# Optimization experiments

Measured on AMD Instinct MI355X. Metric: run time of the kernel, lower is better.

## Reference

```python
import jax, jax.numpy as jnp
import numpy as np

L, H, D, V, CTX = 4, 12, 768, 50257, 2048
HD = D // H
EPS = 1e-5


def setup_inputs() -> dict:
    key = jax.random.key(0)
    ks = jax.random.split(key, 24)
    s = 0.02
    inp = {
        "tokens": jax.random.randint(ks[0], (1, CTX), 0, V, dtype=jnp.int32),
        "vocab_embed": jax.random.normal(ks[1], (V, D), jnp.float32) * s,
        "pos_embed": jax.random.normal(ks[2], (CTX, D), jnp.float32) * s,
        # per-layer stacked params [L, ...]
        "ln1_g": jnp.ones((L, D), jnp.float32),
        "ln1_b": jnp.zeros((L, D), jnp.float32),
        "att_w": jax.random.normal(ks[3], (L, D, 3 * D), jnp.float32) * s,
        "att_b": jnp.zeros((L, 3 * D), jnp.float32),
        "attn_proj_w": jax.random.normal(ks[4], (L, D, D), jnp.float32) * (s / np.sqrt(2 * L)),
        "attn_proj_b": jnp.zeros((L, D), jnp.float32),
        "ln2_g": jnp.ones((L, D), jnp.float32),
        "ln2_b": jnp.zeros((L, D), jnp.float32),
        "fc_w": jax.random.normal(ks[5], (L, D, 4 * D), jnp.float32) * s,
        "fc_b": jnp.zeros((L, 4 * D), jnp.float32),
        "mlp_proj_w": jax.random.normal(ks[6], (L, 4 * D, D), jnp.float32) * (s / np.sqrt(2 * L)),
        "mlp_proj_b": jnp.zeros((L, D), jnp.float32),
        "lnf_g": jnp.ones((D,), jnp.float32),
        "lnf_b": jnp.zeros((D,), jnp.float32),
        "out_w": jax.random.normal(ks[7], (D, V), jnp.float32) * s,
        "out_b": jnp.zeros((V,), jnp.float32),
    }
    return inp


def _layernorm(x, g, b):
    mu = jnp.mean(x, axis=-1, keepdims=True)
    var = jnp.mean(jnp.square(x - mu), axis=-1, keepdims=True)
    return (x - mu) * jax.lax.rsqrt(var + EPS) * g + b


def _gelu(x):
    # exact tanh-approx GELU as in the torch module
    c = np.sqrt(2.0 / np.pi).astype(np.float32)
    return x * 0.5 * (1.0 + jnp.tanh(c * (x + 0.044715 * x * x * x)))


def _forward(tokens, p):
    B, C = tokens.shape
    x = p["vocab_embed"][tokens] + p["pos_embed"][:C][None]  # [B,C,D]
    causal = jnp.tril(jnp.ones((C, C), bool))  # [C,C]
    scale = 1.0 / np.sqrt(HD)
    for l in range(L):
        h = _layernorm(x, p["ln1_g"][l], p["ln1_b"][l])
        qkv = h @ p["att_w"][l] + p["att_b"][l]
        q, k, v = jnp.split(qkv, 3, axis=-1)
        q = q.reshape(B, C, H, HD)
        k = k.reshape(B, C, H, HD)
        v = v.reshape(B, C, H, HD)
        att = jnp.einsum("bqhd,bkhd->bhqk", q, k) * scale
        att = jnp.where(causal[None, None], att, -jnp.inf)
        att = jax.nn.softmax(att, axis=-1)
        o = jnp.einsum("bhqk,bkhd->bqhd", att, v).reshape(B, C, D)
        x = h + (o @ p["attn_proj_w"][l] + p["attn_proj_b"][l])
        h2 = _layernorm(x, p["ln2_g"][l], p["ln2_b"][l])
        mlp = _gelu(h2 @ p["fc_w"][l] + p["fc_b"][l]) @ p["mlp_proj_w"][l] + p["mlp_proj_b"][l]
        x = h2 + mlp
    x = _layernorm(x, p["lnf_g"], p["lnf_b"])
    return x @ p["out_w"] + p["out_b"]  # [B,C,V]


def reference(tokens, vocab_embed, pos_embed, ln1_g, ln1_b, att_w, att_b,
              attn_proj_w, attn_proj_b, ln2_g, ln2_b, fc_w, fc_b,
              mlp_proj_w, mlp_proj_b, lnf_g, lnf_b, out_w, out_b):
    p = dict(vocab_embed=vocab_embed, pos_embed=pos_embed, ln1_g=ln1_g, ln1_b=ln1_b,
             att_w=att_w, att_b=att_b, attn_proj_w=attn_proj_w, attn_proj_b=attn_proj_b,
             ln2_g=ln2_g, ln2_b=ln2_b, fc_w=fc_w, fc_b=fc_b,
             mlp_proj_w=mlp_proj_w, mlp_proj_b=mlp_proj_b,
             lnf_g=lnf_g, lnf_b=lnf_b, out_w=out_w, out_b=out_b)
    return _forward(tokens, p)
```

## Files before the change

kernel.cpp:

```cpp
#include <hip/hip_runtime.h>
#include <hip/hip_bf16.h>
#include <math.h>

#define LAYERS 4
#define NHEAD  12
#define DMODEL 768
#define HEADD  64
#define NCTX   2048
#define NVOCAB 50257
#define NVPAD  50432
#define D3     (3*DMODEL)
#define D4     (4*DMODEL)

typedef short short8 __attribute__((ext_vector_type(8)));
typedef float f32x4  __attribute__((ext_vector_type(4)));
typedef float f32x4u __attribute__((ext_vector_type(4), aligned(4)));
typedef ushort ushx4 __attribute__((ext_vector_type(4)));

__device__ __forceinline__ float bf2f(ushort u) {
    union { uint i; float f; } c; c.i = ((uint)u) << 16; return c.f;
}
__device__ __forceinline__ ushort f2bf(float f) {
    union { float f; uint i; } c; c.f = f;
    uint i = c.i;
    uint r = (i + 0x7FFFu + ((i >> 16) & 1u)) >> 16;
    return (ushort)r;
}

#define GLD16(gp, lp) __builtin_amdgcn_global_load_lds( \
    (__attribute__((address_space(1))) void*)(gp),      \
    (__attribute__((address_space(3))) void*)(lp), 16, 0, 0)

__global__ void embed_k(const int* __restrict__ tok,
                        const float* __restrict__ ve,
                        const float* __restrict__ pe,
                        float* __restrict__ x) {
    int c = blockIdx.x;
    int t = tok[c];
    for (int d = threadIdx.x; d < DMODEL; d += blockDim.x)
        x[(size_t)c * DMODEL + d] = ve[(size_t)t * DMODEL + d] + pe[(size_t)c * DMODEL + d];
}

__global__ __launch_bounds__(256) void ln_v2(const float* __restrict__ x,
                                             const float* __restrict__ g,
                                             const float* __restrict__ b,
                                             float* __restrict__ yf,
                                             ushort* __restrict__ ybf) {
    const int w = threadIdx.x >> 6, l = threadIdx.x & 63;
    const int row = blockIdx.x * 4 + w;
    const float* xr = x + (size_t)row * DMODEL;

    f32x4 v[3];
    float s = 0.f, ss = 0.f;
    #pragma unroll
    for (int i = 0; i < 3; i++) {
        v[i] = *(const f32x4*)(xr + (l + 64 * i) * 4);
        #pragma unroll
        for (int k = 0; k < 4; k++) { s += v[i][k]; ss += v[i][k] * v[i][k]; }
    }
    #pragma unroll
    for (int off = 32; off > 0; off >>= 1) {
        s  += __shfl_xor(s, off);
        ss += __shfl_xor(ss, off);
    }
    const float mu = s * (1.f / DMODEL);
    const float var = ss * (1.f / DMODEL) - mu * mu;
    const float rstd = rsqrtf(var + 1e-5f);

    #pragma unroll
    for (int i = 0; i < 3; i++) {
        const int idx = l + 64 * i;
        f32x4 g4 = *(const f32x4*)(g + idx * 4);
        f32x4 b4 = *(const f32x4*)(b + idx * 4);
        f32x4 r;
        #pragma unroll
        for (int k = 0; k < 4; k++) r[k] = (v[i][k] - mu) * rstd * g4[k] + b4[k];
        if (yf) *(f32x4*)(yf + (size_t)row * DMODEL + idx * 4) = r;
        if (ybf) {
            ushx4 u;
            #pragma unroll
            for (int k = 0; k < 4; k++) u[k] = f2bf(r[k]);
            *(ushx4*)(ybf + (size_t)row * DMODEL + idx * 4) = u;
        }
    }
}

__global__ __launch_bounds__(256) void transp_bf16(const float* __restrict__ src,
                                                   ushort* __restrict__ dst,
                                                   int K, int N) {
    __shared__ float tile[32][33];
    const int nt = blockIdx.x * 32, kt = blockIdx.y * 32;
    const int t = threadIdx.x;
    const int lr = t >> 5, lc = t & 31;

    #pragma unroll
    for (int i = 0; i < 4; i++) {
        int k = kt + lr + i * 8, n = nt + lc;
        float v = (n < N) ? src[(size_t)k * N + n] : 0.f;
        tile[lr + i * 8][lc] = v;
    }
    __syncthreads();
    #pragma unroll
    for (int i = 0; i < 4; i++) {
        int n = nt + lr + i * 8, k = kt + lc;
        dst[(size_t)n * K + k] = f2bf(tile[lc][lr + i * 8]);
    }
}

__global__ __launch_bounds__(256) void transp4(
    const float* __restrict__ s0, const float* __restrict__ s1,
    const float* __restrict__ s2, const float* __restrict__ s3,
    ushort* __restrict__ d0, ushort* __restrict__ d1,
    ushort* __restrict__ d2, ushort* __restrict__ d3)
{
    __shared__ float tile[32][33];
    const int bid = blockIdx.x;
    const float* src; ushort* dst; int K, N, nx, tb;
    if (bid < 1728)      { src = s0; dst = d0; K = 768;  N = 2304; nx = 72; tb = bid; }
    else if (bid < 2304) { src = s1; dst = d1; K = 768;  N = 768;  nx = 24; tb = bid - 1728; }
    else if (bid < 4608) { src = s2; dst = d2; K = 768;  N = 3072; nx = 96; tb = bid - 2304; }
    else                 { src = s3; dst = d3; K = 3072; N = 768;  nx = 24; tb = bid - 4608; }
    const int nt = (tb % nx) * 32, kt = (tb / nx) * 32;
    const int t = threadIdx.x;
    const int lr = t >> 5, lc = t & 31;

    #pragma unroll
    for (int i = 0; i < 4; i++) {
        int k = kt + lr + i * 8, n = nt + lc;
        tile[lr + i * 8][lc] = src[(size_t)k * N + n];
    }
    __syncthreads();
    #pragma unroll
    for (int i = 0; i < 4; i++) {
        int n = nt + lr + i * 8, k = kt + lc;
        dst[(size_t)n * K + k] = f2bf(tile[lc][lr + i * 8]);
    }
}

template<int MT, int ACT, bool HASADD, bool OUTBF>
__global__ __launch_bounds__(256) void gemm3(
    const ushort* __restrict__ A, const ushort* __restrict__ Bt,
    const float* __restrict__ bias, const float* __restrict__ addsrc,
    void* __restrict__ Cout, int N, int K)
{
    constexpr int AFR  = MT / 32;
    constexpr int ABYT = MT * 64;
    constexpr int BUF  = ABYT + 8192;
    constexpr int LPS  = MT / 64 + 2;
    __shared__ __align__(16) char smem[3 * BUF];
    const int bm = blockIdx.y * MT, bn = blockIdx.x * 128;
    const int t = threadIdx.x, l = t & 63, w = t >> 6;
    const int wrb = (w >> 1) * (MT / 2), wcb = (w & 1) * 64;
    const int l15 = l & 15, lg = l >> 4;
    const int swr = ((l15 >> 1) & 3) << 4;

    const int srow = t >> 2;
    const int ssc  = ((t & 3) ^ ((srow >> 1) & 3)) * 8;
    const ushort* Abase = A  + (size_t)(bm + srow) * K + ssc;
    const ushort* Bbase = Bt + (size_t)(bn + srow) * K + ssc;

    f32x4 acc[AFR][4];
    #pragma unroll
    for (int i = 0; i < AFR; i++)
        #pragma unroll
        for (int j = 0; j < 4; j++) acc[i][j] = (f32x4)0.f;

    auto STAGE = [&](int buf, int ke) {
        ushort* as = (ushort*)(smem + buf * BUF);
        ushort* bs = (ushort*)(smem + buf * BUF + ABYT);
        #pragma unroll
        for (int i = 0; i < MT / 64; i++)
            GLD16(Abase + (size_t)i * 64 * K + ke, as + (t + i * 256) * 8);
        #pragma unroll
        for (int i = 0; i < 2; i++)
            GLD16(Bbase + (size_t)i * 64 * K + ke, bs + (t + i * 256) * 8);
    };
    auto COMPUTE = [&](int buf) {
        const char* as = smem + buf * BUF;
        const char* bs = smem + buf * BUF + ABYT;
        short8 af[AFR], bfr[4];
        #pragma unroll
        for (int f = 0; f < AFR; f++)
            af[f] = *(const short8*)(as + (((wrb + f * 16 + l15) * 64 + lg * 16) ^ swr));
        #pragma unroll
        for (int f = 0; f < 4; f++)
            bfr[f] = *(const short8*)(bs + (((wcb + f * 16 + l15) * 64 + lg * 16) ^ swr));
        __builtin_amdgcn_s_setprio(1);
        #pragma unroll
        for (int fm = 0; fm < AFR; fm++)
            #pragma unroll
            for (int fn = 0; fn < 4; fn++)
                acc[fm][fn] = __builtin_amdgcn_mfma_f32_16x16x32_bf16(
                    af[fm], bfr[fn], acc[fm][fn], 0, 0, 0);
        __builtin_amdgcn_s_setprio(0);
    };

    const int nk = K >> 5;
    STAGE(0, 0);
    STAGE(1, 32);
    int bc = 0, bs2 = 2;
    for (int kt = 0; kt < nk; kt++) {
        if (kt < nk - 1)
            asm volatile("s_waitcnt vmcnt(%0)" :: "i"(LPS) : "memory");
        else
            asm volatile("s_waitcnt vmcnt(0)" ::: "memory");
        __builtin_amdgcn_s_barrier();
        asm volatile("" ::: "memory");
        if (kt + 2 < nk) STAGE(bs2, (kt + 2) << 5);
        COMPUTE(bc);
        bc  = (bc  == 2) ? 0 : bc  + 1;
        bs2 = (bs2 == 2) ? 0 : bs2 + 1;
    }

    #pragma unroll
    for (int fn = 0; fn < 4; fn++) {
        const int col = bn + wcb + fn * 16 + l15;
        const float bi = bias[col];
        #pragma unroll
        for (int fm = 0; fm < AFR; fm++) {
            #pragma unroll
            for (int j = 0; j < 4; j++) {
                const int row = bm + wrb + fm * 16 + lg * 4 + j;
                float v = acc[fm][fn][j] + bi;
                if (ACT == 1) {
                    float u = 0.7978845608028654f * (v + 0.044715f * v * v * v);
                    v = 0.5f * v * (1.f + tanhf(u));
                }
                if (HASADD) v += addsrc[(size_t)row * N + col];
                if (OUTBF) ((ushort*)Cout)[(size_t)row * N + col] = f2bf(v);
                else       ((float*) Cout)[(size_t)row * N + col] = v;
            }
        }
    }
}

__global__ __launch_bounds__(1024) void gemm_logits(
    const ushort* __restrict__ A, const ushort* __restrict__ Bt,
    const float* __restrict__ bias, float* __restrict__ Cout)
{
    __shared__ __align__(16) char smem[98304];
    float* Cs = (float*)smem;

    const int pid = (blockIdx.x & 7) * 197 + (blockIdx.x >> 3);
    const int np = pid >> 3, mt = pid & 7;
    const int bm = mt * 256, bn = np * 256;
    const int t = threadIdx.x, l = t & 63, w = t >> 6;
    const int wm = w >> 2, wn = w & 3;
    const int l15 = l & 15, lg = l >> 4;
    const int swr = ((l15 >> 1) & 3) << 4;

    const int sr  = t >> 2;
    const int ssc = ((t & 3) ^ ((sr >> 1) & 3)) * 8;
    const ushort* Ab = A  + (size_t)(bm + sr) * DMODEL + ssc;
    const ushort* Bb = Bt + (size_t)(bn + sr) * DMODEL + ssc;

    f32x4 acc[4][4];
    #pragma unroll
    for (int i = 0; i < 4; i++)
        #pragma unroll
        for (int j = 0; j < 4; j++) acc[i][j] = (f32x4)0.f;

    auto STAGE = [&](int buf, int ke) {
        ushort* as = (ushort*)(smem + buf * 32768);
        ushort* bs = (ushort*)(smem + buf * 32768 + 16384);
        GLD16(Ab + ke, as + t * 8);
        GLD16(Bb + ke, bs + t * 8);
    };
    auto COMPUTE = [&](int buf) {
        const char* as = smem + buf * 32768;
        const char* bs = smem + buf * 32768 + 16384;
        short8 bfr[4];
        #pragma unroll
        for (int f = 0; f < 4; f++) {
            const int r = wn * 64 + f * 16 + l15;
            bfr[f] = *(const short8*)(bs + ((r * 64 + lg * 16) ^ swr));
        }
        __builtin_amdgcn_s_setprio(1);
        #pragma unroll
        for (int fm = 0; fm < 4; fm++) {
            const int r = wm * 64 + fm * 16 + l15;
            short8 af = *(const short8*)(as + ((r * 64 + lg * 16) ^ swr));
            #pragma unroll
            for (int fn = 0; fn < 4; fn++)
                acc[fm][fn] = __builtin_amdgcn_mfma_f32_16x16x32_bf16(
                    af, bfr[fn], acc[fm][fn], 0, 0, 0);
        }
        __builtin_amdgcn_s_setprio(0);
    };

    STAGE(0, 0);
    STAGE(1, 32);
    #pragma unroll
    for (int kt = 0; kt < 24; kt++) {
        if (kt <= 22) asm volatile("s_waitcnt vmcnt(2)" ::: "memory");
        else          asm volatile("s_waitcnt vmcnt(0)" ::: "memory");
        __builtin_amdgcn_s_barrier();
        asm volatile("" ::: "memory");
        if (kt + 2 < 24) STAGE((kt + 2) % 3, (kt + 2) * 32);
        COMPUTE(kt % 3);
    }

    #pragma unroll
    for (int p = 0; p < 4; p++) {
        __syncthreads();
        if (wm == p) {
            #pragma unroll
            for (int fm = 0; fm < 4; fm++) {
                #pragma unroll
                for (int fn = 0; fn < 4; fn++) {
                    const int ccol = wn * 64 + fn * 16 + l15;
                    const int gcol = bn + ccol;
                    const float bi = (gcol < NVOCAB) ? bias[gcol] : 0.f;
                    #pragma unroll
                    for (int j = 0; j < 4; j++)
                        Cs[(fm * 16 + lg * 4 + j) * 256 + ccol] = acc[fm][fn][j] + bi;
                }
            }
        }
        __syncthreads();
        const int grow0 = bm + p * 64;
        #pragma unroll
        for (int i = 0; i < 4; i++) {
            const int idx = t + i * 1024;
            const int rr = idx >> 6, ch = idx & 63;
            f32x4 v = *(const f32x4*)(Cs + rr * 256 + ch * 4);
            float* dst = Cout + (size_t)(grow0 + rr) * NVOCAB + bn + ch * 4;
            if (bn + 256 <= NVOCAB) {
                *(f32x4u*)dst = v;
            } else {
                #pragma unroll
                for (int e = 0; e < 4; e++)
                    if (bn + ch * 4 + e < NVOCAB) dst[e] = v[e];
            }
        }
    }
}

#define QBLK  64
#define KVBLK 64
__global__ __launch_bounds__(256) void qkv_tiles_k(const ushort* __restrict__ qkv,
                                                   ushort* __restrict__ Kimg,
                                                   ushort* __restrict__ Vimg) {
    __shared__ __align__(16) ushort Vt_l[4096];
    const int h = blockIdx.x;
    const int kt = blockIdx.y;
    const int k0 = kt * KVBLK;
    const int t = threadIdx.x;
    ushort* kd = Kimg + ((size_t)h * (NCTX / KVBLK) + kt) * 4096;
    ushort* vd = Vimg + ((size_t)h * (NCTX / KVBLK) + kt) * 4096;

    #pragma unroll
    for (int i = 0; i < 2; i++) {
        const int c = t + i * 256;
        const int r = c >> 3, cc = c & 7;
        short8 kv8 = *(const short8*)(qkv + (size_t)(k0 + r) * D3 + DMODEL + h * HEADD + cc * 8);
        *(short8*)(kd + (((r * 8 + cc) ^ (r & 7)) * 8)) = kv8;
        short8 vv = *(const short8*)(qkv + (size_t)(k0 + r) * D3 + 2 * DMODEL + h * HEADD + cc * 8);
        #pragma unroll
        for (int j = 0; j < 8; j++) {
            const int d = cc * 8 + j;
            const int addr = (d * 128 + r * 2) ^ ((d & 7) << 4);
            *(ushort*)((char*)Vt_l + addr) = (ushort)vv[j];
        }
    }
    __syncthreads();
    #pragma unroll
    for (int i = 0; i < 2; i++) {
        const int c = t + i * 256;
        *(short8*)(vd + c * 8) = *(const short8*)(Vt_l + c * 8);
    }
}

__device__ __forceinline__ void attn_step(
    const short8 qf[2], f32x4 Of[4], float m_run[4], float l_run[4],
    const ushort* Kt, const ushort* Vt, char* pw,
    int k0, int q0, int maskTile, int w, int l15, int lg)
{
    const float scale = 0.125f;
    f32x4 S[4];
    __builtin_amdgcn_s_setprio(1);
    #pragma unroll
    for (int nf = 0; nf < 4; nf++) {
        f32x4 a = (f32x4)0.f;
        #pragma unroll
        for (int s = 0; s < 2; s++) {
            const int r = nf * 16 + l15;
            const int addr = (r * 128 + s * 64 + lg * 16) ^ ((r & 7) << 4);
            short8 kf = *(const short8*)((const char*)Kt + addr);
            a = __builtin_amdgcn_mfma_f32_16x16x32_bf16(qf[s], kf, a, 0, 0, 0);
        }
        S[nf] = a;
    }
    __builtin_amdgcn_s_setprio(0);

    float p[4][4];
    if (maskTile) {
        #pragma unroll
        for (int nf = 0; nf < 4; nf++) {
            const int kvg = k0 + nf * 16 + l15;
            #pragma unroll
            for (int j = 0; j < 4; j++) {
                const int qg = q0 + w * 16 + lg * 4 + j;
                p[nf][j] = (kvg <= qg) ? S[nf][j] * scale : -1e30f;
            }
        }
    } else {
        #pragma unroll
        for (int nf = 0; nf < 4; nf++)
            #pragma unroll
            for (int j = 0; j < 4; j++)
                p[nf][j] = S[nf][j] * scale;
    }

    #pragma unroll
    for (int j = 0; j < 4; j++) {
        float mx = fmaxf(fmaxf(p[0][j], p[1][j]), fmaxf(p[2][j], p[3][j]));
        mx = fmaxf(mx, __shfl_xor(mx, 1));
        mx = fmaxf(mx, __shfl_xor(mx, 2));
        mx = fmaxf(mx, __shfl_xor(mx, 4));
        mx = fmaxf(mx, __shfl_xor(mx, 8));
        const float mnew = fmaxf(m_run[j], mx);
        const float sc = __expf(m_run[j] - mnew);
        m_run[j] = mnew;
        float psum = 0.f;
        #pragma unroll
        for (int nf = 0; nf < 4; nf++) {
            const float e = __expf(p[nf][j] - mnew);
            p[nf][j] = e;
            psum += e;
        }
        psum += __shfl_xor(psum, 1);
        psum += __shfl_xor(psum, 2);
        psum += __shfl_xor(psum, 4);
        psum += __shfl_xor(psum, 8);
        l_run[j] = l_run[j] * sc + psum;
        #pragma unroll
        for (int df = 0; df < 4; df++) Of[df][j] *= sc;
    }

    #pragma unroll
    for (int nf = 0; nf < 4; nf++)
        #pragma unroll
        for (int j = 0; j < 4; j++) {
            const int ql = lg * 4 + j;
            const int addr = (ql * 128 + (nf * 16 + l15) * 2) ^ ((ql & 7) << 4);
            *(ushort*)(pw + addr) = f2bf(p[nf][j]);
        }

    __builtin_amdgcn_s_setprio(1);
    #pragma unroll
    for (int s = 0; s < 2; s++) {
        const int paddr = (l15 * 128 + s * 64 + lg * 16) ^ ((l15 & 7) << 4);
        short8 pf = *(const short8*)(pw + paddr);
        #pragma unroll
        for (int df = 0; df < 4; df++) {
            const int r = df * 16 + l15;
            const int vaddr = (r * 128 + s * 64 + lg * 16) ^ ((r & 7) << 4);
            short8 vf = *(const short8*)((const char*)Vt + vaddr);
            Of[df] = __builtin_amdgcn_mfma_f32_16x16x32_bf16(pf, vf, Of[df], 0, 0, 0);
        }
    }
    __builtin_amdgcn_s_setprio(0);
}

__global__ __launch_bounds__(512) void attn_mfma2(const ushort* __restrict__ qkv,
                                                  const ushort* __restrict__ Kimg,
                                                  const ushort* __restrict__ Vimg,
                                                  ushort* __restrict__ o) {
    const int h   = blockIdx.x;
    const int qaT = blockIdx.y;
    const int qbT = 31 - qaT;
    const int t = threadIdx.x;
    const int w = t >> 6;
    const int strm = w >> 2;
    const int ws = w & 3;
    const int l = t & 63;
    const int l15 = l & 15, lg = l >> 4;

    __shared__ __align__(16) ushort Ks[2][4096];
    __shared__ __align__(16) ushort Vs[2][4096];
    __shared__ __align__(16) ushort Ps[8][1024];

    const int myqT = strm ? qbT : qaT;
    const int q0 = myqT * QBLK;
    const ushort* kbase = Kimg + (size_t)h * (NCTX / KVBLK) * 4096;
    const ushort* vbase = Vimg + (size_t)h * (NCTX / KVBLK) * 4096;
    char* pw = (char*)&Ps[w][0];

    short8 qf[2];
    {
        const int qr = q0 + ws * 16 + l15;
        #pragma unroll
        for (int s = 0; s < 2; s++)
            qf[s] = *(const short8*)(qkv + (size_t)qr * D3 + h * HEADD + s * 32 + lg * 8);
    }

    f32x4 Of[4];
    float m_run[4], l_run[4];
    #pragma unroll
    for (int i = 0; i < 4; i++) {
        Of[i] = (f32x4)0.f;
        m_run[i] = -1e30f; l_run[i] = 0.f;
    }

    const int ntiles = qbT + 1;

    GLD16(kbase + (size_t)t * 8, &Ks[0][t * 8]);
    GLD16(vbase + (size_t)t * 8, &Vs[0][t * 8]);

    for (int kt = 0; kt < ntiles; kt++) {
        const int k0 = kt * KVBLK;
        const int cur = kt & 1;
        __syncthreads();
        if (kt + 1 < ntiles) {
            const ushort* kim = kbase + (size_t)(kt + 1) * 4096;
            const ushort* vim = vbase + (size_t)(kt + 1) * 4096;
            GLD16(kim + (size_t)t * 8, &Ks[cur ^ 1][t * 8]);
            GLD16(vim + (size_t)t * 8, &Vs[cur ^ 1][t * 8]);
        }
        if (kt <= myqT)
            attn_step(qf, Of, m_run, l_run, &Ks[cur][0], &Vs[cur][0], pw,
                      k0, q0, (kt == myqT) ? 1 : 0, ws, l15, lg);
    }

    #pragma unroll
    for (int j = 0; j < 4; j++) {
        const float inv = 1.f / l_run[j];
        const int qg = q0 + ws * 16 + lg * 4 + j;
        #pragma unroll
        for (int df = 0; df < 4; df++)
            o[(size_t)qg * DMODEL + h * HEADD + df * 16 + l15] = f2bf(Of[df][j] * inv);
    }
}

__global__ void layernorm_k(const float* __restrict__ x,
                            const float* __restrict__ g,
                            const float* __restrict__ b,
                            float* __restrict__ y) {
    const int row = blockIdx.x;
    const float* xr = x + (size_t)row * DMODEL;
    __shared__ float red[256];
    const int tid = threadIdx.x;
    float s = 0.f;
    for (int d = tid; d < DMODEL; d += 256) s += xr[d];
    red[tid] = s; __syncthreads();
    for (int off = 128; off > 0; off >>= 1) {
        if (tid < off) red[tid] += red[tid + off];
        __syncthreads();
    }
    const float mu = red[0] / DMODEL;
    __syncthreads();
    float v = 0.f;
    for (int d = tid; d < DMODEL; d += 256) { float tv = xr[d] - mu; v += tv * tv; }
    red[tid] = v; __syncthreads();
    for (int off = 128; off > 0; off >>= 1) {
        if (tid < off) red[tid] += red[tid + off];
        __syncthreads();
    }
    const float rstd = rsqrtf(red[0] / DMODEL + 1e-5f);
    for (int d = tid; d < DMODEL; d += 256)
        y[(size_t)row * DMODEL + d] = (xr[d] - mu) * rstd * g[d] + b[d];
}

#define BM 64
#define BN 64
#define BK 16
__global__ __launch_bounds__(256)
void gemm_f32(const float* __restrict__ A, const float* __restrict__ B,
              const float* __restrict__ bias, const float* __restrict__ addsrc,
              float* __restrict__ C, int M, int N, int K, int act) {
    __shared__ float As[BK][BM];
    __shared__ float Bs[BK][BN];
    const int bm = blockIdx.y * BM;
    const int bn = blockIdx.x * BN;
    const int tid = threadIdx.x;
    const int tr = tid >> 4;
    const int tc = tid & 15;
    float acc[4][4] = {};
    for (int k0 = 0; k0 < K; k0 += BK) {
        #pragma unroll
        for (int i = 0; i < 4; i++) {
            int idx = tid + i * 256;
            int row = idx >> 4, col = idx & 15;
            int gm = bm + row;
            float v = 0.f;
            if (gm < M) v = A[(size_t)gm * K + (k0 + col)];
            As[col][row] = v;
        }
        #pragma unroll
        for (int i = 0; i < 4; i++) {
            int idx = tid + i * 256;
            int row = idx >> 6, col = idx & 63;
            int gn = bn + col;
            float v = 0.f;
            if (gn < N) v = B[(size_t)(k0 + row) * N + gn];
            Bs[row][col] = v;
        }
        __syncthreads();
        #pragma unroll
        for (int kk = 0; kk < BK; kk++) {
            float a[4], bb[4];
            #pragma unroll
            for (int i = 0; i < 4; i++) a[i] = As[kk][tr * 4 + i];
            #pragma unroll
            for (int j = 0; j < 4; j++) bb[j] = Bs[kk][tc * 4 + j];
            #pragma unroll
            for (int i = 0; i < 4; i++)
                #pragma unroll
                for (int j = 0; j < 4; j++)
                    acc[i][j] += a[i] * bb[j];
        }
        __syncthreads();
    }
    #pragma unroll
    for (int i = 0; i < 4; i++) {
        int gm = bm + tr * 4 + i;
        if (gm >= M) continue;
        #pragma unroll
        for (int j = 0; j < 4; j++) {
            int gn = bn + tc * 4 + j;
            if (gn >= N) continue;
            float v = acc[i][j] + (bias ? bias[gn] : 0.f);
            if (act == 1) {
                const float cst = 0.7978845608028654f;
                float tt = tanhf(cst * (v + 0.044715f * v * v * v));
                v = 0.5f * v * (1.f + tt);
            }
            if (addsrc) v += addsrc[(size_t)gm * N + gn];
            C[(size_t)gm * N + gn] = v;
        }
    }
}

__global__ __launch_bounds__(256)
void attn_k(const float* __restrict__ qkv, float* __restrict__ o) {
    const int q = blockIdx.x;
    const int h = blockIdx.y;
    const int tid = threadIdx.x;
    __shared__ float qrow[HEADD];
    __shared__ float sc[NCTX];
    __shared__ float red[256];
    __shared__ float part[4][HEADD];
    if (tid < HEADD) qrow[tid] = qkv[(size_t)q * D3 + h * HEADD + tid];
    __syncthreads();
    const float scale = 0.125f;
    float lmax = -1e30f;
    for (int k = tid; k <= q; k += 256) {
        const float* kr = qkv + (size_t)k * D3 + DMODEL + h * HEADD;
        float s = 0.f;
        #pragma unroll
        for (int d = 0; d < HEADD; d++) s += qrow[d] * kr[d];
        s *= scale;
        sc[k] = s;
        lmax = fmaxf(lmax, s);
    }
    red[tid] = lmax; __syncthreads();
    for (int off = 128; off > 0; off >>= 1) {
        if (tid < off) red[tid] = fmaxf(red[tid], red[tid + off]);
        __syncthreads();
    }
    const float m = red[0];
    __syncthreads();
    float lsum = 0.f;
    for (int k = tid; k <= q; k += 256) {
        float p = expf(sc[k] - m);
        sc[k] = p;
        lsum += p;
    }
    red[tid] = lsum; __syncthreads();
    for (int off = 128; off > 0; off >>= 1) {
        if (tid < off) red[tid] += red[tid + off];
        __syncthreads();
    }
    const float inv = 1.f / red[0];
    const int grp = tid >> 6;
    const int d = tid & 63;
    float acc = 0.f;
    for (int k = grp; k <= q; k += 4)
        acc += sc[k] * qkv[(size_t)k * D3 + 2 * DMODEL + h * HEADD + d];
    part[grp][d] = acc;
    __syncthreads();
    if (tid < HEADD) {
        float v = (part[0][tid] + part[1][tid] + part[2][tid] + part[3][tid]) * inv;
        o[(size_t)q * DMODEL + h * HEADD + tid] = v;
    }
}

extern "C" void kernel_launch(void* const* d_in, const int* in_sizes, int n_in,
                              void* d_out, int out_size, void* d_ws, size_t ws_size,
                              hipStream_t stream) {
    const int*   tokens      = (const int*)  d_in[0];
    const float* vocab_embed = (const float*)d_in[1];
    const float* pos_embed   = (const float*)d_in[2];
    const float* ln1_g       = (const float*)d_in[3];
    const float* ln1_b       = (const float*)d_in[4];
    const float* att_w       = (const float*)d_in[5];
    const float* att_b       = (const float*)d_in[6];
    const float* attn_proj_w = (const float*)d_in[7];
    const float* attn_proj_b = (const float*)d_in[8];
    const float* ln2_g       = (const float*)d_in[9];
    const float* ln2_b       = (const float*)d_in[10];
    const float* fc_w        = (const float*)d_in[11];
    const float* fc_b        = (const float*)d_in[12];
    const float* mlp_proj_w  = (const float*)d_in[13];
    const float* mlp_proj_b  = (const float*)d_in[14];
    const float* lnf_g       = (const float*)d_in[15];
    const float* lnf_b       = (const float*)d_in[16];
    const float* out_w       = (const float*)d_in[17];
    const float* out_b       = (const float*)d_in[18];
    float* out = (float*)d_out;

    const int C = NCTX;
    dim3 blk(256);

    char* wp = (char*)d_ws;
    size_t used = 0;
    auto carve = [&](size_t bytes) -> void* {
        bytes = (bytes + 255) & ~(size_t)255;
        void* p = wp + used;
        used += bytes;
        return p;
    };
    float*  x_f    = (float*) carve((size_t)C * DMODEL * 4);
    float*  h_f    = (float*) carve((size_t)C * DMODEL * 4);
    ushort* h_bf   = (ushort*)carve((size_t)C * DMODEL * 2);
    ushort* qkv_bf = (ushort*)carve((size_t)C * D3 * 2);
    ushort* o_bf   = (ushort*)carve((size_t)C * DMODEL * 2);
    ushort* mid_bf = (ushort*)carve((size_t)C * D4 * 2);
    ushort* wt_a   = (ushort*)carve((size_t)D3 * DMODEL * 2);
    ushort* wt_p   = (ushort*)carve((size_t)DMODEL * DMODEL * 2);
    ushort* wt_f   = (ushort*)carve((size_t)D4 * DMODEL * 2);
    ushort* wt_m   = (ushort*)carve((size_t)DMODEL * D4 * 2);
    ushort* wt_out = (ushort*)carve((size_t)NVPAD * DMODEL * 2);
    ushort* Kimg   = (ushort*)carve((size_t)NHEAD * (C / KVBLK) * 4096 * 2);
    ushort* Vimg   = (ushort*)carve((size_t)NHEAD * (C / KVBLK) * 4096 * 2);

    if (ws_size >= used) {
        transp_bf16<<<dim3(NVPAD / 32, DMODEL / 32), blk, 0, stream>>>(
            out_w, wt_out, DMODEL, NVOCAB);

        embed_k<<<dim3(C), blk, 0, stream>>>(tokens, vocab_embed, pos_embed, x_f);

        for (int l = 0; l < LAYERS; l++) {
            transp4<<<dim3(6912), blk, 0, stream>>>(
                att_w + (size_t)l * DMODEL * D3,
                attn_proj_w + (size_t)l * DMODEL * DMODEL,
                fc_w + (size_t)l * DMODEL * D4,
                mlp_proj_w + (size_t)l * D4 * DMODEL,
                wt_a, wt_p, wt_f, wt_m);

            ln_v2<<<dim3(C / 4), blk, 0, stream>>>(
                x_f, ln1_g + l * DMODEL, ln1_b + l * DMODEL, h_f, h_bf);

            gemm3<128, 0, false, true><<<dim3(D3 / 128, C / 128), blk, 0, stream>>>(
                h_bf, wt_a, att_b + l * D3, nullptr, qkv_bf, D3, DMODEL);

            qkv_tiles_k<<<dim3(NHEAD, C / KVBLK), blk, 0, stream>>>(qkv_bf, Kimg, Vimg);

            attn_mfma2<<<dim3(NHEAD, 16), dim3(512), 0, stream>>>(qkv_bf, Kimg, Vimg, o_bf);

            gemm3<64, 0, true, false><<<dim3(DMODEL / 128, C / 64), blk, 0, stream>>>(
                o_bf, wt_p, attn_proj_b + l * DMODEL, h_f, x_f, DMODEL, DMODEL);

            ln_v2<<<dim3(C / 4), blk, 0, stream>>>(
                x_f, ln2_g + l * DMODEL, ln2_b + l * DMODEL, h_f, h_bf);

            gemm3<128, 1, false, true><<<dim3(D4 / 128, C / 128), blk, 0, stream>>>(
                h_bf, wt_f, fc_b + l * D4, nullptr, mid_bf, D4, DMODEL);

            gemm3<64, 0, true, false><<<dim3(DMODEL / 128, C / 64), blk, 0, stream>>>(
                mid_bf, wt_m, mlp_proj_b + l * DMODEL, h_f, x_f, DMODEL, D4);
        }

        ln_v2<<<dim3(C / 4), blk, 0, stream>>>(x_f, lnf_g, lnf_b, nullptr, h_bf);

        gemm_logits<<<dim3(1576), dim3(1024), 0, stream>>>(h_bf, wt_out, out_b, out);
        return;
    }

    const size_t n_x   = (size_t)C * DMODEL;
    const size_t n_qkv = (size_t)C * D3;
    const size_t need_bytes = (3 * n_x + n_qkv + (size_t)C * D4) * sizeof(float);

    float *x, *h, *o, *qkv, *mid;
    float* ws = (float*)d_ws;
    if (ws_size >= need_bytes) {
        x = ws; h = x + n_x; o = h + n_x; qkv = o + n_x; mid = qkv + n_qkv;
    } else {
        x = ws; h = x + n_x; o = h + n_x;
        qkv = (float*)d_out; mid = qkv + n_qkv;
    }

    embed_k<<<dim3(C), blk, 0, stream>>>(tokens, vocab_embed, pos_embed, x);
    for (int l = 0; l < LAYERS; l++) {
        const float* lw;
        layernorm_k<<<dim3(C), blk, 0, stream>>>(x, ln1_g + l * DMODEL, ln1_b + l * DMODEL, h);
        lw = att_w + (size_t)l * DMODEL * D3;
        gemm_f32<<<dim3(D3 / BN, C / BM), blk, 0, stream>>>(
            h, lw, att_b + l * D3, nullptr, qkv, C, D3, DMODEL, 0);
        attn_k<<<dim3(C, NHEAD), blk, 0, stream>>>(qkv, o);
        lw = attn_proj_w + (size_t)l * DMODEL * DMODEL;
        gemm_f32<<<dim3(DMODEL / BN, C / BM), blk, 0, stream>>>(
            o, lw, attn_proj_b + l * DMODEL, h, x, C, DMODEL, DMODEL, 0);
        layernorm_k<<<dim3(C), blk, 0, stream>>>(x, ln2_g + l * DMODEL, ln2_b + l * DMODEL, h);
        lw = fc_w + (size_t)l * DMODEL * D4;
        gemm_f32<<<dim3(D4 / BN, C / BM), blk, 0, stream>>>(
            h, lw, fc_b + l * D4, nullptr, mid, C, D4, DMODEL, 1);
        lw = mlp_proj_w + (size_t)l * D4 * DMODEL;
        gemm_f32<<<dim3(DMODEL / BN, C / BM), blk, 0, stream>>>(
            mid, lw, mlp_proj_b + l * DMODEL, h, x, C, DMODEL, D4, 0);
    }
    layernorm_k<<<dim3(C), blk, 0, stream>>>(x, lnf_g, lnf_b, h);
    gemm_f32<<<dim3((NVOCAB + BN - 1) / BN, C / BM), blk, 0, stream>>>(
        h, out_w, out_b, nullptr, out, C, NVOCAB, DMODEL, 0);
}
```

Baseline: 983.8 us.

## Double K-depth logits GEMM tiles and split attention into per-query-tile blocks

The logits GEMM now stages 64-wide K slices with 128-byte swizzled rows into two 64KB buffers. This replaces the previous 32-wide triple buffer and halves the number of barrier iterations, at the cost of 128KB of LDS and a full vmcnt(0) wait each step. The attention kernel no longer pairs a short and a long query tile in one 512-thread block. It launches one 256-thread block per query tile, with longest tiles first, trading the paired load balance for more, smaller blocks.

```diff
diff --git a/kernel.cpp b/kernel.cpp
--- a/kernel.cpp
+++ b/kernel.cpp
@@ -30,6 +30,9 @@
 #define GLD16(gp, lp) __builtin_amdgcn_global_load_lds( \
     (__attribute__((address_space(1))) void*)(gp),      \
     (__attribute__((address_space(3))) void*)(lp), 16, 0, 0)
+
+#define BARS() do { asm volatile("s_waitcnt vmcnt(0)" ::: "memory"); \
+                    __builtin_amdgcn_s_barrier(); } while (0)
 
 __global__ void embed_k(const int* __restrict__ tok,
                         const float* __restrict__ ve,
@@ -238,7 +241,7 @@
     const ushort* __restrict__ A, const ushort* __restrict__ Bt,
     const float* __restrict__ bias, float* __restrict__ Cout)
 {
-    __shared__ __align__(16) char smem[98304];
+    __shared__ __align__(16) char smem[131072];
     float* Cs = (float*)smem;
 
     const int pid = (blockIdx.x & 7) * 197 + (blockIdx.x >> 3);
@@ -247,10 +250,9 @@
     const int t = threadIdx.x, l = t & 63, w = t >> 6;
     const int wm = w >> 2, wn = w & 3;
     const int l15 = l & 15, lg = l >> 4;
-    const int swr = ((l15 >> 1) & 3) << 4;
-
-    const int sr  = t >> 2;
-    const int ssc = ((t & 3) ^ ((sr >> 1) & 3)) * 8;
+
+    const int sr  = t >> 3;
+    const int ssc = ((t & 7) ^ (sr & 7)) * 8;
     const ushort* Ab = A  + (size_t)(bm + sr) * DMODEL + ssc;
     const ushort* Bb = Bt + (size_t)(bn + sr) * DMODEL + ssc;
 
@@ -261,43 +263,46 @@
         for (int j = 0; j < 4; j++) acc[i][j] = (f32x4)0.f;
 
     auto STAGE = [&](int buf, int ke) {
-        ushort* as = (ushort*)(smem + buf * 32768);
-        ushort* bs = (ushort*)(smem + buf * 32768 + 16384);
+        ushort* as = (ushort*)(smem + buf * 65536);
+        ushort* bs = (ushort*)(smem + buf * 65536 + 32768);
         GLD16(Ab + ke, as + t * 8);
+        GLD16(Ab + (size_t)128 * DMODEL + ke, as + (t + 1024) * 8);
         GLD16(Bb + ke, bs + t * 8);
+        GLD16(Bb + (size_t)128 * DMODEL + ke, bs + (t + 1024) * 8);
     };
     auto COMPUTE = [&](int buf) {
-        const char* as = smem + buf * 32768;
-        const char* bs = smem + buf * 32768 + 16384;
-        short8 bfr[4];
-        #pragma unroll
-        for (int f = 0; f < 4; f++) {
-            const int r = wn * 64 + f * 16 + l15;
-            bfr[f] = *(const short8*)(bs + ((r * 64 + lg * 16) ^ swr));
-        }
-        __builtin_amdgcn_s_setprio(1);
-        #pragma unroll
-        for (int fm = 0; fm < 4; fm++) {
-            const int r = wm * 64 + fm * 16 + l15;
-            short8 af = *(const short8*)(as + ((r * 64 + lg * 16) ^ swr));
-            #pragma unroll
-            for (int fn = 0; fn < 4; fn++)
-                acc[fm][fn] = __builtin_amdgcn_mfma_f32_16x16x32_bf16(
-                    af, bfr[fn], acc[fm][fn], 0, 0, 0);
-        }
-        __builtin_amdgcn_s_setprio(0);
+        const char* as = smem + buf * 65536;
+        const char* bs = smem + buf * 65536 + 32768;
+        #pragma unroll
+        for (int s = 0; s < 2; s++) {
+            short8 bfr[4];
+            #pragma unroll
+            for (int f = 0; f < 4; f++) {
+                const int r = wn * 64 + f * 16 + l15;
+                bfr[f] = *(const short8*)(bs +
+                          ((r * 128 + s * 64 + lg * 16) ^ ((r & 7) << 4)));
+            }
+            __builtin_amdgcn_s_setprio(1);
+            #pragma unroll
+            for (int fm = 0; fm < 4; fm++) {
+                const int r = wm * 64 + fm * 16 + l15;
+                short8 af = *(const short8*)(as +
+                             ((r * 128 + s * 64 + lg * 16) ^ ((r & 7) << 4)));
+                #pragma unroll
+                for (int fn = 0; fn < 4; fn++)
+                    acc[fm][fn] = __builtin_amdgcn_mfma_f32_16x16x32_bf16(
+                        af, bfr[fn], acc[fm][fn], 0, 0, 0);
+            }
+            __builtin_amdgcn_s_setprio(0);
+        }
     };
 
     STAGE(0, 0);
-    STAGE(1, 32);
-    #pragma unroll
-    for (int kt = 0; kt < 24; kt++) {
-        if (kt <= 22) asm volatile("s_waitcnt vmcnt(2)" ::: "memory");
-        else          asm volatile("s_waitcnt vmcnt(0)" ::: "memory");
-        __builtin_amdgcn_s_barrier();
-        asm volatile("" ::: "memory");
-        if (kt + 2 < 24) STAGE((kt + 2) % 3, (kt + 2) * 32);
-        COMPUTE(kt % 3);
+    #pragma unroll
+    for (int kt = 0; kt < 12; kt++) {
+        BARS();
+        if (kt + 1 < 12) STAGE((kt + 1) & 1, (kt + 1) * 64);
+        COMPUTE(kt & 1);
     }
 
     #pragma unroll
@@ -463,33 +468,29 @@
     __builtin_amdgcn_s_setprio(0);
 }
 
-__global__ __launch_bounds__(512) void attn_mfma2(const ushort* __restrict__ qkv,
+__global__ __launch_bounds__(256) void attn_mfma3(const ushort* __restrict__ qkv,
                                                   const ushort* __restrict__ Kimg,
                                                   const ushort* __restrict__ Vimg,
                                                   ushort* __restrict__ o) {
-    const int h   = blockIdx.x;
-    const int qaT = blockIdx.y;
-    const int qbT = 31 - qaT;
+    const int h  = blockIdx.x;
+    const int qT = 31 - (int)blockIdx.y;
+    const int q0 = qT * QBLK;
     const int t = threadIdx.x;
     const int w = t >> 6;
-    const int strm = w >> 2;
-    const int ws = w & 3;
     const int l = t & 63;
     const int l15 = l & 15, lg = l >> 4;
 
     __shared__ __align__(16) ushort Ks[2][4096];
     __shared__ __align__(16) ushort Vs[2][4096];
-    __shared__ __align__(16) ushort Ps[8][1024];
-
-    const int myqT = strm ? qbT : qaT;
-    const int q0 = myqT * QBLK;
+    __shared__ __align__(16) ushort Ps[4][1024];
+
     const ushort* kbase = Kimg + (size_t)h * (NCTX / KVBLK) * 4096;
     const ushort* vbase = Vimg + (size_t)h * (NCTX / KVBLK) * 4096;
     char* pw = (char*)&Ps[w][0];
 
     short8 qf[2];
     {
-        const int qr = q0 + ws * 16 + l15;
+        const int qr = q0 + w * 16 + l15;
         #pragma unroll
         for (int s = 0; s < 2; s++)
             qf[s] = *(const short8*)(qkv + (size_t)qr * D3 + h * HEADD + s * 32 + lg * 8);
@@ -503,10 +504,13 @@
         m_run[i] = -1e30f; l_run[i] = 0.f;
     }
 
-    const int ntiles = qbT + 1;
-
-    GLD16(kbase + (size_t)t * 8, &Ks[0][t * 8]);
-    GLD16(vbase + (size_t)t * 8, &Vs[0][t * 8]);
+    const int ntiles = qT + 1;
+
+    #pragma unroll
+    for (int i = 0; i < 2; i++) {
+        GLD16(kbase + (size_t)(t + i * 256) * 8, &Ks[0][(t + i * 256) * 8]);
+        GLD16(vbase + (size_t)(t + i * 256) * 8, &Vs[0][(t + i * 256) * 8]);
+    }
 
     for (int kt = 0; kt < ntiles; kt++) {
         const int k0 = kt * KVBLK;
@@ -515,18 +519,20 @@
         if (kt + 1 < ntiles) {
             const ushort* kim = kbase + (size_t)(kt + 1) * 4096;
             const ushort* vim = vbase + (size_t)(kt + 1) * 4096;
-            GLD16(kim + (size_t)t * 8, &Ks[cur ^ 1][t * 8]);
-            GLD16(vim + (size_t)t * 8, &Vs[cur ^ 1][t * 8]);
-        }
-        if (kt <= myqT)
-            attn_step(qf, Of, m_run, l_run, &Ks[cur][0], &Vs[cur][0], pw,
-                      k0, q0, (kt == myqT) ? 1 : 0, ws, l15, lg);
+            #pragma unroll
+            for (int i = 0; i < 2; i++) {
+                GLD16(kim + (size_t)(t + i * 256) * 8, &Ks[cur ^ 1][(t + i * 256) * 8]);
+                GLD16(vim + (size_t)(t + i * 256) * 8, &Vs[cur ^ 1][(t + i * 256) * 8]);
+            }
+        }
+        attn_step(qf, Of, m_run, l_run, &Ks[cur][0], &Vs[cur][0], pw,
+                  k0, q0, (kt == qT) ? 1 : 0, w, l15, lg);
     }
 
     #pragma unroll
     for (int j = 0; j < 4; j++) {
         const float inv = 1.f / l_run[j];
-        const int qg = q0 + ws * 16 + lg * 4 + j;
+        const int qg = q0 + w * 16 + lg * 4 + j;
         #pragma unroll
         for (int df = 0; df < 4; df++)
             o[(size_t)qg * DMODEL + h * HEADD + df * 16 + l15] = f2bf(Of[df][j] * inv);
@@ -757,7 +763,7 @@
 
             qkv_tiles_k<<<dim3(NHEAD, C / KVBLK), blk, 0, stream>>>(qkv_bf, Kimg, Vimg);
 
-            attn_mfma2<<<dim3(NHEAD, 16), dim3(512), 0, stream>>>(qkv_bf, Kimg, Vimg, o_bf);
+            attn_mfma3<<<dim3(NHEAD, 32), blk, 0, stream>>>(qkv_bf, Kimg, Vimg, o_bf);
 
             gemm3<64, 0, true, false><<<dim3(DMODEL / 128, C / 64), blk, 0, stream>>>(
                 o_bf, wt_p, attn_proj_b + l * DMODEL, h_f, x_f, DMODEL, DMODEL);
```

Result: slower. 1.022 ms (+3.9%).
